# Optimization experiments

Measured on AMD Instinct MI355X. Metric: run time of the kernel, lower is better.

Reference implementation:

```python
import jax, jax.numpy as jnp
import numpy as np

EPS = 1e-8  # matches torch F.cosine_similarity eps


def setup_inputs() -> dict:
    key = jax.random.key(0)
    S, U, D = 2048, 10, 256  # speakers, utterances/speaker, embedding dim
    embeddings = jax.random.normal(key, (S * U, D), dtype=jnp.float32)
    labels = jnp.repeat(jnp.arange(S, dtype=jnp.int64), U)  # speaker-blocked, as the view() assumes
    return {"embeddings": embeddings, "labels": labels}


def reference(embeddings, labels):
    labels_np = np.asarray(labels)
    S = int(np.unique(labels_np).size)          # num_speakers (static)
    B, D = embeddings.shape
    U = B // S                                   # num_utterances
    E = embeddings.reshape(S, U, D)
    C = E.mean(axis=1)                           # (S, D) centroids
    En = E / jnp.maximum(jnp.linalg.norm(E, axis=-1, keepdims=True), EPS)
    Cn = C / jnp.maximum(jnp.linalg.norm(C, axis=-1, keepdims=True), EPS)
    sim = jnp.einsum('sud,kd->suk', En, Cn)      # (S, U, S) cosine similarities
    idx = jnp.arange(S)
    pos = sim[idx, :, idx]                       # (S, U) similarity to own centroid
    neg_mask = jnp.eye(S, dtype=bool)[:, None, :]  # mask out k == i
    neg = jnp.where(neg_mask, -jnp.inf, sim)
    lse = jax.nn.logsumexp(neg, axis=-1)         # (S, U)
    loss = jnp.mean(-pos + lse)
    return loss
```

## Files before the change

kernel.cpp:

```cpp
#include <hip/hip_runtime.h>
#include <math.h>

#define SS   2048
#define UU   10
#define DD   256
#define BB   (SS * UU)
#define EPSF 1e-8f

typedef __attribute__((ext_vector_type(8))) short   bf16x8;
typedef __attribute__((ext_vector_type(4))) float   floatx4;

__device__ static inline unsigned short f2bf(float f) {
    union { float f; unsigned u; } v; v.f = f;
    unsigned r = (v.u + 0x7FFFu + ((v.u >> 16) & 1u)) >> 16;
    return (unsigned short)r;
}

__device__ static inline void gl_lds16(const unsigned short* g, unsigned short* l) {
    __builtin_amdgcn_global_load_lds((const __attribute__((address_space(1))) void*)g,
                                     (__attribute__((address_space(3))) void*)l, 16, 0, 0);
}

#define NORM_NBLK (BB / 4)
#define CENT_NBLK (SS / 4)

__global__ __launch_bounds__(256) void prep_kernel(const float* __restrict__ E,
                                                   unsigned short* __restrict__ Enb,
                                                   unsigned short* __restrict__ Cnb,
                                                   float* __restrict__ sumexp,
                                                   float* __restrict__ out) {
    const int wid = threadIdx.x >> 6, lane = threadIdx.x & 63;
    const int b = blockIdx.x;

    if (b < NORM_NBLK) {
        const int row = b * 4 + wid;
        const float4 v = ((const float4*)(E + (size_t)row * DD))[lane];
        float ssq = v.x * v.x + v.y * v.y + v.z * v.z + v.w * v.w;
#pragma unroll
        for (int off = 32; off; off >>= 1) ssq += __shfl_xor(ssq, off, 64);
        const float rinv = 1.0f / fmaxf(sqrtf(ssq), EPSF);
        ushort4 o;
        o.x = f2bf(v.x * rinv); o.y = f2bf(v.y * rinv);
        o.z = f2bf(v.z * rinv); o.w = f2bf(v.w * rinv);
        ((ushort4*)(Enb + (size_t)row * DD))[lane] = o;
        if (lane == 0) {
            sumexp[row] = 0.f;
            if (row == 0) out[0] = 0.f;
        }
    } else {
        const int s = (b - NORM_NBLK) * 4 + wid;
        const float* base = E + (size_t)s * UU * DD + lane * 4;
        float4 c = {0.f, 0.f, 0.f, 0.f};
#pragma unroll
        for (int u = 0; u < UU; ++u) {
            const float4 v = *(const float4*)(base + u * DD);
            c.x += v.x; c.y += v.y; c.z += v.z; c.w += v.w;
        }
        c.x *= 0.1f; c.y *= 0.1f; c.z *= 0.1f; c.w *= 0.1f;
        float ssq = c.x * c.x + c.y * c.y + c.z * c.z + c.w * c.w;
#pragma unroll
        for (int off = 32; off; off >>= 1) ssq += __shfl_xor(ssq, off, 64);
        const float rinv = 1.0f / fmaxf(sqrtf(ssq), EPSF);
        ushort4 o;
        o.x = f2bf(c.x * rinv); o.y = f2bf(c.y * rinv);
        o.z = f2bf(c.z * rinv); o.w = f2bf(c.w * rinv);
        ((ushort4*)(Cnb + (size_t)s * DD))[lane] = o;
    }
}

#define BM 128
#define BN 128
#define BK 32

__global__ __launch_bounds__(256) void gemm_lse_kernel(const unsigned short* __restrict__ Enb,
                                                       const unsigned short* __restrict__ Cnb,
                                                       float* __restrict__ posArr,
                                                       float* __restrict__ sumexp) {
    __shared__ unsigned short As[BM * BK];
    __shared__ unsigned short Bs[BN * BK];

    const int tid  = threadIdx.x;
    const int wid  = tid >> 6, lane = tid & 63;
    const int l15  = lane & 15, quad = lane >> 4;
    const int wave_m = wid >> 1, wave_n = wid & 1;

    const int bn = blockIdx.x & 15;
    const int bm = blockIdx.x >> 4;
    const int row0 = bm * BM, n0 = bn * BN;

    const int rl = lane >> 2;
    const int gf = ((lane & 3) ^ ((rl >> 1) & 3)) * 8;
    const unsigned short* gp[4];
    unsigned short* lp[4];
#pragma unroll
    for (int i = 0; i < 4; ++i) {
        const int c = wid * 4 + i;
        if (c < 8) {
            gp[i] = Enb + (size_t)(row0 + c * 16 + rl) * DD + gf;
            lp[i] = As + c * 512;
        } else {
            gp[i] = Cnb + (size_t)(n0 + (c - 8) * 16 + rl) * DD + gf;
            lp[i] = Bs + (c - 8) * 512;
        }
    }

    const int fswz = (quad ^ ((l15 >> 1) & 3)) * 8;
    int aoff[4], boff[4];
#pragma unroll
    for (int t = 0; t < 4; ++t) {
        aoff[t] = (wave_m * 64 + t * 16 + l15) * BK + fswz;
        boff[t] = (wave_n * 64 + t * 16 + l15) * BK + fswz;
    }

    floatx4 acc[4][4];
#pragma unroll
    for (int i = 0; i < 4; ++i)
#pragma unroll
        for (int j = 0; j < 4; ++j) acc[i][j] = (floatx4){0.f, 0.f, 0.f, 0.f};

    for (int k0 = 0; k0 < DD; k0 += BK) {
        __syncthreads();
#pragma unroll
        for (int i = 0; i < 4; ++i) gl_lds16(gp[i] + k0, lp[i]);
        __syncthreads();

        bf16x8 af[4], bfr[4];
#pragma unroll
        for (int t = 0; t < 4; ++t) af[t]  = *(const bf16x8*)(As + aoff[t]);
#pragma unroll
        for (int t = 0; t < 4; ++t) bfr[t] = *(const bf16x8*)(Bs + boff[t]);
#pragma unroll
        for (int mt = 0; mt < 4; ++mt)
#pragma unroll
            for (int nt = 0; nt < 4; ++nt)
                acc[mt][nt] = __builtin_amdgcn_mfma_f32_16x16x32_bf16(af[mt], bfr[nt], acc[mt][nt], 0, 0, 0);
    }

#pragma unroll
    for (int mt = 0; mt < 4; ++mt) {
        float rs[4] = {0.f, 0.f, 0.f, 0.f};
        const int growb = row0 + wave_m * 64 + mt * 16 + quad * 4;
#pragma unroll
        for (int nt = 0; nt < 4; ++nt) {
            const int col = n0 + wave_n * 64 + nt * 16 + l15;
#pragma unroll
            for (int r = 0; r < 4; ++r) {
                const int grow = growb + r;
                const float sim = acc[mt][nt][r];
                if (col == grow / UU) {
                    posArr[grow] = sim;
                } else {
                    rs[r] += __expf(sim);
                }
            }
        }
#pragma unroll
        for (int m = 1; m < 16; m <<= 1) {
#pragma unroll
            for (int r = 0; r < 4; ++r) rs[r] += __shfl_xor(rs[r], m, 64);
        }
        if (l15 == 0) {
#pragma unroll
            for (int r = 0; r < 4; ++r) atomicAdd(&sumexp[growb + r], rs[r]);
        }
    }
}

__global__ __launch_bounds__(256) void finalize_kernel(const float* __restrict__ posArr,
                                                       const float* __restrict__ sumexp,
                                                       float* __restrict__ out) {
    __shared__ float sred[256];
    const int tid = threadIdx.x;
    const int r = blockIdx.x * 256 + tid;
    sred[tid] = __logf(sumexp[r]) - posArr[r];
    __syncthreads();
#pragma unroll
    for (int off = 128; off; off >>= 1) {
        if (tid < off) sred[tid] += sred[tid + off];
        __syncthreads();
    }
    if (tid == 0) atomicAdd(out, sred[0] * (1.0f / (float)BB));
}

extern "C" void kernel_launch(void* const* d_in, const int* in_sizes, int n_in,
                              void* d_out, int out_size, void* d_ws, size_t ws_size,
                              hipStream_t stream) {
    const float* E = (const float*)d_in[0];
    float* out = (float*)d_out;

    unsigned short* Enb = (unsigned short*)d_ws;
    unsigned short* Cnb = Enb + (size_t)BB * DD;
    float* posArr = (float*)(Cnb + (size_t)SS * DD);
    float* sumexp = posArr + BB;

    prep_kernel<<<NORM_NBLK + CENT_NBLK, 256, 0, stream>>>(E, Enb, Cnb, sumexp, out);
    gemm_lse_kernel<<<(BB / BM) * (SS / BN), 256, 0, stream>>>(Enb, Cnb, posArr, sumexp);
    finalize_kernel<<<BB / 256, 256, 0, stream>>>(posArr, sumexp, out);
}
```

Before: 116.4 us.

## Restructure GEMM-LSE with resident A tile, per-wave pipelined B, fused finalize

Each block now keeps a full 64x256 slice of normalized embeddings in LDS. Each of its four waves streams its own 128 centroid columns through a private triple-buffered LDS ring, using explicit vmcnt waits in place of block-wide barriers. The exp-sum epilogue runs after every 64-column group and resets the accumulators. The separate finalize kernel is replaced by a per-row-block arrival counter, so the last-arriving wave reduces log-sum-exp minus the positive term into the output. This removes a kernel launch and the per-k-step block synchronization, at the cost of larger LDS use, more atomics and a leftover redundant A-fragment load.

New measurement: 208.9 us. 1.79x slower.

```diff
diff --git a/kernel.cpp b/kernel.cpp
--- a/kernel.cpp
+++ b/kernel.cpp
@@ -23,16 +23,19 @@
 
 #define NORM_NBLK (BB / 4)
 #define CENT_NBLK (SS / 4)
+#define NBM       320
 
 __global__ __launch_bounds__(256) void prep_kernel(const float* __restrict__ E,
                                                    unsigned short* __restrict__ Enb,
                                                    unsigned short* __restrict__ Cnb,
                                                    float* __restrict__ sumexp,
+                                                   int* __restrict__ cnt,
                                                    float* __restrict__ out) {
     const int wid = threadIdx.x >> 6, lane = threadIdx.x & 63;
     const int b = blockIdx.x;
 
     if (b < NORM_NBLK) {
+        if (b < NBM && threadIdx.x == 0) cnt[b] = 0;
         const int row = b * 4 + wid;
         const float4 v = ((const float4*)(E + (size_t)row * DD))[lane];
         float ssq = v.x * v.x + v.y * v.y + v.z * v.z + v.w * v.w;
@@ -68,118 +71,144 @@
     }
 }
 
-#define BM 128
-#define BN 128
-#define BK 32
-
-__global__ __launch_bounds__(256) void gemm_lse_kernel(const unsigned short* __restrict__ Enb,
-                                                       const unsigned short* __restrict__ Cnb,
-                                                       float* __restrict__ posArr,
-                                                       float* __restrict__ sumexp) {
-    __shared__ unsigned short As[BM * BK];
-    __shared__ unsigned short Bs[BN * BK];
+__global__ __launch_bounds__(256, 2) void gemm_lse_kernel(const unsigned short* __restrict__ Enb,
+                                                          const unsigned short* __restrict__ Cnb,
+                                                          float* __restrict__ posArr,
+                                                          float* __restrict__ sumexp,
+                                                          int* __restrict__ cnt,
+                                                          float* __restrict__ out) {
+    __shared__ unsigned short As[64 * 256];
+    __shared__ unsigned short Bs[4][3][2048];
 
     const int tid  = threadIdx.x;
     const int wid  = tid >> 6, lane = tid & 63;
     const int l15  = lane & 15, quad = lane >> 4;
-    const int wave_m = wid >> 1, wave_n = wid & 1;
-
-    const int bn = blockIdx.x & 15;
-    const int bm = blockIdx.x >> 4;
-    const int row0 = bm * BM, n0 = bn * BN;
+
+    const int q  = blockIdx.x & 3;
+    const int bm = blockIdx.x >> 2;
+    const int row0 = bm * 64;
+    const int c0   = q * 512 + wid * 128;
+
+    {
+        const int rl2 = lane >> 5;
+        const int sl2 = lane & 31;
+#pragma unroll
+        for (int i = 0; i < 8; ++i) {
+            const int ci  = wid * 8 + i;
+            const int row = ci * 2 + rl2;
+            const int g   = sl2 ^ (row & 7);
+            gl_lds16(Enb + (size_t)(row0 + row) * DD + g * 8, As + ci * 512);
+        }
+    }
 
     const int rl = lane >> 2;
-    const int gf = ((lane & 3) ^ ((rl >> 1) & 3)) * 8;
-    const unsigned short* gp[4];
-    unsigned short* lp[4];
-#pragma unroll
-    for (int i = 0; i < 4; ++i) {
-        const int c = wid * 4 + i;
-        if (c < 8) {
-            gp[i] = Enb + (size_t)(row0 + c * 16 + rl) * DD + gf;
-            lp[i] = As + c * 512;
+    const int gfb = ((lane & 3) ^ ((rl >> 1) & 3)) * 8;
+#pragma unroll
+    for (int t = 0; t < 2; ++t) {
+#pragma unroll
+        for (int i = 0; i < 4; ++i) {
+            const int colg = c0 + (t >> 3) * 64 + i * 16 + rl;
+            gl_lds16(Cnb + (size_t)colg * DD + (t & 7) * 32 + gfb,
+                     &Bs[wid][t % 3][i * 512]);
+        }
+    }
+
+    __syncthreads();
+
+    const int bswz = (quad ^ ((l15 >> 1) & 3)) * 8;
+    const int aswz = quad ^ (l15 & 7);
+    int arow[4];
+#pragma unroll
+    for (int mt = 0; mt < 4; ++mt) arow[mt] = (mt * 16 + l15) * 256;
+
+    floatx4 acc[4][4];
+#pragma unroll
+    for (int i = 0; i < 4; ++i)
+#pragma unroll
+        for (int j = 0; j < 4; ++j) acc[i][j] = (floatx4){0.f, 0.f, 0.f, 0.f};
+
+#pragma unroll
+    for (int s = 0; s < 16; ++s) {
+        if (s < 14) {
+            const int t = s + 2;
+#pragma unroll
+            for (int i = 0; i < 4; ++i) {
+                const int colg = c0 + (t >> 3) * 64 + i * 16 + rl;
+                gl_lds16(Cnb + (size_t)colg * DD + (t & 7) * 32 + gfb,
+                         &Bs[wid][t % 3][i * 512]);
+            }
+            asm volatile("s_waitcnt vmcnt(8)" ::: "memory");
+        } else if (s == 14) {
+            asm volatile("s_waitcnt vmcnt(4)" ::: "memory");
         } else {
-            gp[i] = Cnb + (size_t)(n0 + (c - 8) * 16 + rl) * DD + gf;
-            lp[i] = Bs + (c - 8) * 512;
-        }
-    }
-
-    const int fswz = (quad ^ ((l15 >> 1) & 3)) * 8;
-    int aoff[4], boff[4];
-#pragma unroll
-    for (int t = 0; t < 4; ++t) {
-        aoff[t] = (wave_m * 64 + t * 16 + l15) * BK + fswz;
-        boff[t] = (wave_n * 64 + t * 16 + l15) * BK + fswz;
-    }
-
-    floatx4 acc[4][4];
-#pragma unroll
-    for (int i = 0; i < 4; ++i)
-#pragma unroll
-        for (int j = 0; j < 4; ++j) acc[i][j] = (floatx4){0.f, 0.f, 0.f, 0.f};
-
-    for (int k0 = 0; k0 < DD; k0 += BK) {
-        __syncthreads();
-#pragma unroll
-        for (int i = 0; i < 4; ++i) gl_lds16(gp[i] + k0, lp[i]);
-        __syncthreads();
-
+            asm volatile("s_waitcnt vmcnt(0)" ::: "memory");
+        }
+
+        const int ks = s & 7;
         bf16x8 af[4], bfr[4];
 #pragma unroll
-        for (int t = 0; t < 4; ++t) af[t]  = *(const bf16x8*)(As + aoff[t]);
-#pragma unroll
-        for (int t = 0; t < 4; ++t) bfr[t] = *(const bf16x8*)(Bs + boff[t]);
+        for (int mt = 0; mt < 4; ++mt)
+            af[mt] = *(const bf16x8*)(As + arow[mt] + ((ks * 4) ^ aswz) * 8
+                                      + (((ks * 4) ^ aswz) >= ((ks * 4 + quad) ^ aswz) ? 0 : 0));
+#pragma unroll
+        for (int mt = 0; mt < 4; ++mt)
+            af[mt] = *(const bf16x8*)(As + arow[mt] + (((ks * 4 + quad) ^ (l15 & 7)) * 8));
+#pragma unroll
+        for (int nt = 0; nt < 4; ++nt)
+            bfr[nt] = *(const bf16x8*)(&Bs[wid][s % 3][(nt * 16 + l15) * 32 + bswz]);
 #pragma unroll
         for (int mt = 0; mt < 4; ++mt)
 #pragma unroll
             for (int nt = 0; nt < 4; ++nt)
                 acc[mt][nt] = __builtin_amdgcn_mfma_f32_16x16x32_bf16(af[mt], bfr[nt], acc[mt][nt], 0, 0, 0);
-    }
-
-#pragma unroll
-    for (int mt = 0; mt < 4; ++mt) {
-        float rs[4] = {0.f, 0.f, 0.f, 0.f};
-        const int growb = row0 + wave_m * 64 + mt * 16 + quad * 4;
-#pragma unroll
-        for (int nt = 0; nt < 4; ++nt) {
-            const int col = n0 + wave_n * 64 + nt * 16 + l15;
-#pragma unroll
-            for (int r = 0; r < 4; ++r) {
-                const int grow = growb + r;
-                const float sim = acc[mt][nt][r];
-                if (col == grow / UU) {
-                    posArr[grow] = sim;
-                } else {
-                    rs[r] += __expf(sim);
+
+        if (ks == 7) {
+            const int cbase = c0 + (s >> 3) * 64;
+#pragma unroll
+            for (int mt = 0; mt < 4; ++mt) {
+                float rs[4] = {0.f, 0.f, 0.f, 0.f};
+                const int growb = row0 + mt * 16 + quad * 4;
+#pragma unroll
+                for (int nt = 0; nt < 4; ++nt) {
+                    const int col = cbase + nt * 16 + l15;
+#pragma unroll
+                    for (int r = 0; r < 4; ++r) {
+                        const int grow = growb + r;
+                        const float sim = acc[mt][nt][r];
+                        if (col == grow / UU) {
+                            posArr[grow] = sim;
+                        } else {
+                            rs[r] += __expf(sim);
+                        }
+                        acc[mt][nt][r] = 0.f;
+                    }
+                }
+#pragma unroll
+                for (int m = 1; m < 16; m <<= 1) {
+#pragma unroll
+                    for (int r = 0; r < 4; ++r) rs[r] += __shfl_xor(rs[r], m, 64);
+                }
+                if (l15 == 0) {
+#pragma unroll
+                    for (int r = 0; r < 4; ++r) atomicAdd(&sumexp[growb + r], rs[r]);
                 }
             }
         }
-#pragma unroll
-        for (int m = 1; m < 16; m <<= 1) {
-#pragma unroll
-            for (int r = 0; r < 4; ++r) rs[r] += __shfl_xor(rs[r], m, 64);
-        }
-        if (l15 == 0) {
-#pragma unroll
-            for (int r = 0; r < 4; ++r) atomicAdd(&sumexp[growb + r], rs[r]);
-        }
-    }
-}
-
-__global__ __launch_bounds__(256) void finalize_kernel(const float* __restrict__ posArr,
-                                                       const float* __restrict__ sumexp,
-                                                       float* __restrict__ out) {
-    __shared__ float sred[256];
-    const int tid = threadIdx.x;
-    const int r = blockIdx.x * 256 + tid;
-    sred[tid] = __logf(sumexp[r]) - posArr[r];
-    __syncthreads();
-#pragma unroll
-    for (int off = 128; off; off >>= 1) {
-        if (tid < off) sred[tid] += sred[tid + off];
-        __syncthreads();
-    }
-    if (tid == 0) atomicAdd(out, sred[0] * (1.0f / (float)BB));
+    }
+
+    __threadfence();
+    int old = 0;
+    if (lane == 0) old = atomicAdd(&cnt[bm], 1);
+    old = __shfl(old, 0, 64);
+    if (old == 15) {
+        __threadfence();
+        const float se = atomicAdd(&sumexp[row0 + lane], 0.0f);
+        const float ps = atomicAdd(&posArr[row0 + lane], 0.0f);
+        float t = __logf(se) - ps;
+#pragma unroll
+        for (int off = 32; off; off >>= 1) t += __shfl_xor(t, off, 64);
+        if (lane == 0) atomicAdd(out, t * (1.0f / (float)BB));
+    }
 }
 
 extern "C" void kernel_launch(void* const* d_in, const int* in_sizes, int n_in,
@@ -192,8 +221,8 @@
     unsigned short* Cnb = Enb + (size_t)BB * DD;
     float* posArr = (float*)(Cnb + (size_t)SS * DD);
     float* sumexp = posArr + BB;
-
-    prep_kernel<<<NORM_NBLK + CENT_NBLK, 256, 0, stream>>>(E, Enb, Cnb, sumexp, out);
-    gemm_lse_kernel<<<(BB / BM) * (SS / BN), 256, 0, stream>>>(Enb, Cnb, posArr, sumexp);
-    finalize_kernel<<<BB / 256, 256, 0, stream>>>(posArr, sumexp, out);
-}
+    int*   cnt    = (int*)(sumexp + BB);
+
+    prep_kernel<<<NORM_NBLK + CENT_NBLK, 256, 0, stream>>>(E, Enb, Cnb, sumexp, cnt, out);
+    gemm_lse_kernel<<<NBM * 4, 256, 0, stream>>>(Enb, Cnb, posArr, sumexp, cnt, out);
+}
```

## Double-buffer GEMM tiles via register prefetch and fuse finalize via last-block counter

Applied to the files above, without the earlier changes.

Replaces the direct global-to-LDS loads and two barriers per K step with a register-staged, double-buffered LDS pipeline that prefetches two K slices ahead, so global load latency overlaps the MFMA work. It also removes the separate finalize kernel. The 16th block to finish a row tile, detected with a per-tile atomic counter reset in prep, computes log-sum-exp minus the positive similarity for that tile and adds it to the output. This saves one kernel launch, at the cost of doubled LDS, more live registers, and a threadfence plus atomic at the end of every block.

New measurement: 453.7 us. +289.8%, slower.

```diff
diff --git a/kernel.cpp b/kernel.cpp
--- a/kernel.cpp
+++ b/kernel.cpp
@@ -16,10 +16,10 @@
     return (unsigned short)r;
 }
 
-__device__ static inline void gl_lds16(const unsigned short* g, unsigned short* l) {
-    __builtin_amdgcn_global_load_lds((const __attribute__((address_space(1))) void*)g,
-                                     (__attribute__((address_space(3))) void*)l, 16, 0, 0);
-}
+#define BM 128
+#define BN 128
+#define BK 32
+#define NBM2 (BB / BM)
 
 #define NORM_NBLK (BB / 4)
 #define CENT_NBLK (SS / 4)
@@ -28,11 +28,13 @@
                                                    unsigned short* __restrict__ Enb,
                                                    unsigned short* __restrict__ Cnb,
                                                    float* __restrict__ sumexp,
+                                                   int* __restrict__ cnt,
                                                    float* __restrict__ out) {
     const int wid = threadIdx.x >> 6, lane = threadIdx.x & 63;
     const int b = blockIdx.x;
 
     if (b < NORM_NBLK) {
+        if (b < NBM2 && threadIdx.x == 0) cnt[b] = 0;
         const int row = b * 4 + wid;
         const float4 v = ((const float4*)(E + (size_t)row * DD))[lane];
         float ssq = v.x * v.x + v.y * v.y + v.z * v.z + v.w * v.w;
@@ -68,16 +70,14 @@
     }
 }
 
-#define BM 128
-#define BN 128
-#define BK 32
-
 __global__ __launch_bounds__(256) void gemm_lse_kernel(const unsigned short* __restrict__ Enb,
                                                        const unsigned short* __restrict__ Cnb,
                                                        float* __restrict__ posArr,
-                                                       float* __restrict__ sumexp) {
-    __shared__ unsigned short As[BM * BK];
-    __shared__ unsigned short Bs[BN * BK];
+                                                       float* __restrict__ sumexp,
+                                                       int* __restrict__ cnt,
+                                                       float* __restrict__ out) {
+    __shared__ unsigned short L[2][(BM + BN) * BK];
+    __shared__ int lastflag;
 
     const int tid  = threadIdx.x;
     const int wid  = tid >> 6, lane = tid & 63;
@@ -91,17 +91,13 @@
     const int rl = lane >> 2;
     const int gf = ((lane & 3) ^ ((rl >> 1) & 3)) * 8;
     const unsigned short* gp[4];
-    unsigned short* lp[4];
+    int lo[4];
 #pragma unroll
     for (int i = 0; i < 4; ++i) {
         const int c = wid * 4 + i;
-        if (c < 8) {
-            gp[i] = Enb + (size_t)(row0 + c * 16 + rl) * DD + gf;
-            lp[i] = As + c * 512;
-        } else {
-            gp[i] = Cnb + (size_t)(n0 + (c - 8) * 16 + rl) * DD + gf;
-            lp[i] = Bs + (c - 8) * 512;
-        }
+        gp[i] = (c < 8) ? Enb + (size_t)(row0 + c * 16 + rl) * DD + gf
+                        : Cnb + (size_t)(n0 + (c - 8) * 16 + rl) * DD + gf;
+        lo[i] = c * 512 + lane * 8;
     }
 
     const int fswz = (quad ^ ((l15 >> 1) & 3)) * 8;
@@ -109,8 +105,17 @@
 #pragma unroll
     for (int t = 0; t < 4; ++t) {
         aoff[t] = (wave_m * 64 + t * 16 + l15) * BK + fswz;
-        boff[t] = (wave_n * 64 + t * 16 + l15) * BK + fswz;
-    }
+        boff[t] = BM * BK + (wave_n * 64 + t * 16 + l15) * BK + fswz;
+    }
+
+    uint4 g[2][4];
+#pragma unroll
+    for (int i = 0; i < 4; ++i) g[0][i] = *(const uint4*)(gp[i]);
+#pragma unroll
+    for (int i = 0; i < 4; ++i) g[1][i] = *(const uint4*)(gp[i] + 32);
+#pragma unroll
+    for (int i = 0; i < 4; ++i) *(uint4*)&L[0][lo[i]] = g[0][i];
+    asm volatile("s_waitcnt lgkmcnt(0)\n\ts_barrier" ::: "memory");
 
     floatx4 acc[4][4];
 #pragma unroll
@@ -118,22 +123,28 @@
 #pragma unroll
         for (int j = 0; j < 4; ++j) acc[i][j] = (floatx4){0.f, 0.f, 0.f, 0.f};
 
-    for (int k0 = 0; k0 < DD; k0 += BK) {
-        __syncthreads();
-#pragma unroll
-        for (int i = 0; i < 4; ++i) gl_lds16(gp[i] + k0, lp[i]);
-        __syncthreads();
-
+#pragma unroll
+    for (int s = 0; s < 8; ++s) {
+        if (s < 6) {
+#pragma unroll
+            for (int i = 0; i < 4; ++i) g[s & 1][i] = *(const uint4*)(gp[i] + (s + 2) * 32);
+        }
+        const unsigned short* Lc = L[s & 1];
         bf16x8 af[4], bfr[4];
 #pragma unroll
-        for (int t = 0; t < 4; ++t) af[t]  = *(const bf16x8*)(As + aoff[t]);
-#pragma unroll
-        for (int t = 0; t < 4; ++t) bfr[t] = *(const bf16x8*)(Bs + boff[t]);
+        for (int t = 0; t < 4; ++t) af[t]  = *(const bf16x8*)(Lc + aoff[t]);
+#pragma unroll
+        for (int t = 0; t < 4; ++t) bfr[t] = *(const bf16x8*)(Lc + boff[t]);
 #pragma unroll
         for (int mt = 0; mt < 4; ++mt)
 #pragma unroll
             for (int nt = 0; nt < 4; ++nt)
                 acc[mt][nt] = __builtin_amdgcn_mfma_f32_16x16x32_bf16(af[mt], bfr[nt], acc[mt][nt], 0, 0, 0);
+        if (s < 7) {
+#pragma unroll
+            for (int i = 0; i < 4; ++i) *(uint4*)&L[(s + 1) & 1][lo[i]] = g[(s + 1) & 1][i];
+            asm volatile("s_waitcnt lgkmcnt(0)\n\ts_barrier" ::: "memory");
+        }
     }
 
 #pragma unroll
@@ -164,22 +175,24 @@
             for (int r = 0; r < 4; ++r) atomicAdd(&sumexp[growb + r], rs[r]);
         }
     }
-}
-
-__global__ __launch_bounds__(256) void finalize_kernel(const float* __restrict__ posArr,
-                                                       const float* __restrict__ sumexp,
-                                                       float* __restrict__ out) {
-    __shared__ float sred[256];
-    const int tid = threadIdx.x;
-    const int r = blockIdx.x * 256 + tid;
-    sred[tid] = __logf(sumexp[r]) - posArr[r];
+
+    __threadfence();
     __syncthreads();
-#pragma unroll
-    for (int off = 128; off; off >>= 1) {
-        if (tid < off) sred[tid] += sred[tid + off];
-        __syncthreads();
-    }
-    if (tid == 0) atomicAdd(out, sred[0] * (1.0f / (float)BB));
+    if (tid == 0) lastflag = (atomicAdd(&cnt[bm], 1) == 15);
+    __syncthreads();
+    if (lastflag) {
+        __threadfence();
+        float t = 0.f;
+        if (tid < BM) {
+            const int r = row0 + tid;
+            const float se = atomicAdd(&sumexp[r], 0.0f);
+            const float ps = atomicAdd(&posArr[r], 0.0f);
+            t = __logf(se) - ps;
+        }
+#pragma unroll
+        for (int off = 32; off; off >>= 1) t += __shfl_xor(t, off, 64);
+        if (lane == 0 && tid < BM) atomicAdd(out, t * (1.0f / (float)BB));
+    }
 }
 
 extern "C" void kernel_launch(void* const* d_in, const int* in_sizes, int n_in,
@@ -192,8 +205,8 @@
     unsigned short* Cnb = Enb + (size_t)BB * DD;
     float* posArr = (float*)(Cnb + (size_t)SS * DD);
     float* sumexp = posArr + BB;
-
-    prep_kernel<<<NORM_NBLK + CENT_NBLK, 256, 0, stream>>>(E, Enb, Cnb, sumexp, out);
-    gemm_lse_kernel<<<(BB / BM) * (SS / BN), 256, 0, stream>>>(Enb, Cnb, posArr, sumexp);
-    finalize_kernel<<<BB / 256, 256, 0, stream>>>(posArr, sumexp, out);
-}
+    int*   cnt    = (int*)(sumexp + BB);
+
+    prep_kernel<<<NORM_NBLK + CENT_NBLK, 256, 0, stream>>>(E, Enb, Cnb, sumexp, cnt, out);
+    gemm_lse_kernel<<<NBM2 * 16, 256, 0, stream>>>(Enb, Cnb, posArr, sumexp, cnt, out);
+}
```
